# Optimization experiments

Hardware: AMD Instinct MI355X
Metric: run time of the kernel (lower is better)

## Reference

```python
import jax, jax.numpy as jnp
import numpy as np


def patch_merge(x):
    # [B,C,H,W] -> [B,4C,H/2,W/2], channel order [x00, x10, x01, x11]
    x0 = x[:, :, 0::2, 0::2]
    x1 = x[:, :, 1::2, 0::2]
    x2 = x[:, :, 0::2, 1::2]
    x3 = x[:, :, 1::2, 1::2]
    return jnp.concatenate([x0, x1, x2, x3], axis=1)


def patch2image(x):
    # inverse of patch_merge: [B,4C,H,W] -> [B,C,2H,2W]
    B, C4, H, W = x.shape
    C = C4 // 4
    a, b, c, d = x[:, :C], x[:, C:2 * C], x[:, 2 * C:3 * C], x[:, 3 * C:]
    even = jnp.stack([a, c], axis=-1).reshape(B, C, H, 2 * W)  # rows 0::2
    odd = jnp.stack([b, d], axis=-1).reshape(B, C, H, 2 * W)   # rows 1::2
    return jnp.stack([even, odd], axis=-2).reshape(B, C, 2 * H, 2 * W)


def dwconv3x3(x, w, b):
    # depthwise 3x3 conv, SAME padding; w: [C,1,3,3], b: [C]
    C = x.shape[1]
    y = jax.lax.conv_general_dilated(
        x, w, window_strides=(1, 1), padding='SAME',
        dimension_numbers=('NCHW', 'OIHW', 'NCHW'), feature_group_count=C)
    return y + b[None, :, None, None]


def setup_inputs() -> dict:
    key = jax.random.key(0)
    ks = jax.random.split(key, 6)
    B, C, H, W = 8, 32, 256, 256
    x = jax.random.normal(ks[0], (B, C, H, W), dtype=jnp.float32)
    wq = jax.random.normal(ks[1], (C, 1, 3, 3), dtype=jnp.float32) * 0.1
    bq = jax.random.normal(ks[2], (C,), dtype=jnp.float32) * 0.1
    wk = jax.random.normal(ks[3], (C, 1, 3, 3), dtype=jnp.float32) * 0.1
    bk = jax.random.normal(ks[4], (C,), dtype=jnp.float32) * 0.1
    w1 = jax.random.normal(ks[5], (C, C), dtype=jnp.float32) * 0.1  # 1x1 conv, no bias
    return {'x': x, 'wq': wq, 'bq': bq, 'wk': wk, 'bk': bk, 'w1': w1}


def reference(x, wq, bq, wk, bk, w1):
    Q = dwconv3x3(x, wq, bq)
    K = dwconv3x3(x, wk, bk)
    V = x
    for _ in range(4):
        Q = patch_merge(Q)
        K = patch_merge(K)
        V = patch_merge(V)
    b, c, h, w = V.shape
    Qf = Q.reshape(b, c, h * w)
    Kf = K.reshape(b, c, h * w)
    Vf = V.reshape(b, c, h * w)
    # S[b,i,j] = sum_c Q[b,c,i] K[b,c,j]; softmax over j (dim=2)
    S = jax.nn.softmax(jnp.einsum('bci,bcj->bij', Qf, Kf), axis=2)
    # E = V @ S^T
    E = jnp.einsum('bcj,bij->bci', Vf, S).reshape(b, c, h, w)
    for _ in range(4):
        E = patch2image(E)
    E = E + x
    return jnp.einsum('oi,bihw->bohw', w1, E)
```

## Files before the change

### kernel.cpp

```cpp
#include <hip/hip_runtime.h>

#define B_ 8
#define C_ 32
#define NI 256
#define C4 8192

typedef _Float16 f16;
typedef __attribute__((ext_vector_type(8))) _Float16 f16x8;
typedef __attribute__((ext_vector_type(4))) _Float16 f16x4;
typedef __attribute__((ext_vector_type(2))) _Float16 f16x2;
typedef __attribute__((ext_vector_type(4))) float f32x4;

__device__ __forceinline__ int dh_of(int t) { return (t & 1) | ((t >> 1) & 2) | ((t >> 2) & 4) | ((t >> 3) & 8); }
__device__ __forceinline__ int dw_of(int t) { return ((t >> 1) & 1) | ((t >> 2) & 2) | ((t >> 3) & 4) | ((t >> 4) & 8); }
__device__ __forceinline__ int swzu(int u) { return u ^ ((u >> 3) & 7); }

__device__ __forceinline__ void gld16(const void* g, void* lds) {
  __builtin_amdgcn_global_load_lds(
      (const __attribute__((address_space(1))) unsigned int*)g,
      (__attribute__((address_space(3))) unsigned int*)lds, 16, 0, 0);
}

__global__ __launch_bounds__(256) void k1a_conv(
    const float* __restrict__ x, const float* __restrict__ wq, const float* __restrict__ bq,
    const float* __restrict__ wk, const float* __restrict__ bk,
    f16* __restrict__ Qn, f16* __restrict__ Kn, f16* __restrict__ Vtt)
{
  __shared__ __align__(16) float xs[19 * 260];
  const int bid = blockIdx.x;
  const int hi = bid & 15, c = (bid >> 4) & 31, b = bid >> 9;
  const int tid = threadIdx.x;
  const size_t cimg = ((size_t)(b * 32 + c)) << 16;

  if (tid < 19) {
    f32x4 z = {};
    *(f32x4*)&xs[tid * 260 + 256] = z;
  }
#pragma unroll
  for (int s = 0; s < 5; ++s) {
    const int idx = tid + 256 * s;
    if (idx < 1152) {
      const int rr = idx >> 6;
      const int col4 = idx & 63;
      const int gh = hi * 16 - 1 + rr;
      f32x4 v = {};
      if ((unsigned)gh < 256u)
        v = *(const f32x4*)(x + cimg + (size_t)gh * 256 + col4 * 4);
      *(f32x4*)&xs[(rr + 1) * 260 + (swzu(col4) << 2)] = v;
    }
  }
  __syncthreads();

  {
    const int hl = tid >> 4, wseg = tid & 15;
    const int w0 = wseg * 16;
    const int ubase = 4 * wseg - 1;
    float q[16], k[16];
    const float bqv = bq[c], bkv = bk[c];
#pragma unroll
    for (int w = 0; w < 16; ++w) { q[w] = bqv; k[w] = bkv; }
#pragma unroll
    for (int dy = 0; dy < 3; ++dy) {
      const float* row = &xs[(hl + 1 + dy) * 260];
      float rbuf[24];
#pragma unroll
      for (int v6 = 0; v6 < 6; ++v6) {
        const int u = ubase + v6;
        const int off = (u < 0) ? -4 : (u >= 64 ? 256 : (swzu(u) << 2));
        const f32x4 a = *(const f32x4*)(row + off);
#pragma unroll
        for (int e = 0; e < 4; ++e) rbuf[v6 * 4 + e] = a[e];
      }
      const float q0 = wq[c * 9 + dy * 3], q1 = wq[c * 9 + dy * 3 + 1], q2 = wq[c * 9 + dy * 3 + 2];
      const float k0 = wk[c * 9 + dy * 3], k1 = wk[c * 9 + dy * 3 + 1], k2 = wk[c * 9 + dy * 3 + 2];
#pragma unroll
      for (int w = 0; w < 16; ++w) {
        q[w] += rbuf[3 + w] * q0 + rbuf[4 + w] * q1 + rbuf[5 + w] * q2;
        k[w] += rbuf[3 + w] * k0 + rbuf[4 + w] * k1 + rbuf[5 + w] * k2;
      }
    }
    f16x8 qo[2], ko[2];
#pragma unroll
    for (int w = 0; w < 16; ++w) { qo[w >> 3][w & 7] = (f16)q[w]; ko[w >> 3][w & 7] = (f16)k[w]; }
    f16* qp = Qn + cimg + (size_t)(hi * 16 + hl) * 256 + w0;
    f16* kp = Kn + cimg + (size_t)(hi * 16 + hl) * 256 + w0;
    *(f16x8*)qp = qo[0]; *(f16x8*)(qp + 8) = qo[1];
    *(f16x8*)kp = ko[0]; *(f16x8*)(kp + 8) = ko[1];
  }

  {
    const int t = tid;
    const int dh = dh_of(t), dw = dw_of(t);
    const float* rowp = &xs[(dh + 2) * 260];
    f16x8 o0, o1;
#pragma unroll
    for (int wi = 0; wi < 16; ++wi) {
      const int wcol = wi * 16 + dw;
      const f16 v = (f16)rowp[(swzu(wcol >> 2) << 2) | (wcol & 3)];
      if (wi < 8) o0[wi] = v; else o1[wi - 8] = v;
    }
    f16* vdst = Vtt + ((size_t)b * C4 + (size_t)t * 32 + c) * 256 + hi * 16;
    *(f16x8*)vdst = o0;
    *(f16x8*)(vdst + 8) = o1;
  }
}

__global__ __launch_bounds__(256) void k2_logits(
    const f16* __restrict__ Qn, const f16* __restrict__ Kn, float* __restrict__ Spart)
{
  const int b = blockIdx.z;
  const int kt = blockIdx.y;
  const int it = blockIdx.x >> 2, jt = blockIdx.x & 3;
  const int tid = threadIdx.x, wave = tid >> 6, lane = tid & 63;
  const int li = lane & 15, lk = lane >> 4;
  const int i0 = it * 64 + wave * 16;
  const int j0 = jt * 64;
  const f16* Qb = Qn + ((size_t)b << 21);
  const f16* Kb = Kn + ((size_t)b << 21);
  const int dhl = lk >> 1, dwl = (lk & 1) * 8;

  f32x4 acc[4] = {};
  const int kbeg = kt * 2048, kend = kbeg + 2048;
  for (int kk = kbeg; kk < kend; kk += 32) {
    const int c = kk >> 8, dhb = (kk >> 4) & 15;
    const size_t cbase = ((size_t)c << 16) + (size_t)(dhb + dhl) * 256 + li * 16 + dwl;
    const f16x8 a = *(const f16x8*)(Qb + cbase + (size_t)i0 * 256);
#pragma unroll
    for (int jj = 0; jj < 4; ++jj) {
      const f16x8 bb = *(const f16x8*)(Kb + cbase + (size_t)(j0 + jj * 16) * 256);
      acc[jj] = __builtin_amdgcn_mfma_f32_16x16x32_f16(a, bb, acc[jj], 0, 0, 0);
    }
  }
  float* Sp = Spart + ((size_t)kt * B_ + b) * NI * NI;
#pragma unroll
  for (int jj = 0; jj < 4; ++jj)
#pragma unroll
    for (int r = 0; r < 4; ++r) {
      const int ii = i0 + lk * 4 + r;
      const int jc = j0 + jj * 16 + li;
      Sp[(size_t)ii * NI + jc] = acc[jj][r];
    }
}

__global__ __launch_bounds__(256) void k3_softmax(
    const float* __restrict__ Spart, f16* __restrict__ Sh)
{
  const int row = blockIdx.x * 4 + (threadIdx.x >> 6);
  const int lane = threadIdx.x & 63;
  const size_t base = (size_t)row * NI + lane * 4;
  f32x4 v = {0.f, 0.f, 0.f, 0.f};
#pragma unroll
  for (int kt = 0; kt < 4; ++kt) {
    const f32x4 p = *(const f32x4*)(Spart + (size_t)kt * B_ * NI * NI + base);
    v[0] += p[0]; v[1] += p[1]; v[2] += p[2]; v[3] += p[3];
  }
  float m = fmaxf(fmaxf(v[0], v[1]), fmaxf(v[2], v[3]));
#pragma unroll
  for (int d = 1; d < 64; d <<= 1) m = fmaxf(m, __shfl_xor(m, d, 64));
  const float e0 = expf(v[0] - m), e1 = expf(v[1] - m), e2 = expf(v[2] - m), e3 = expf(v[3] - m);
  float s = e0 + e1 + e2 + e3;
#pragma unroll
  for (int d = 1; d < 64; d <<= 1) s += __shfl_xor(s, d, 64);
  const float inv = 1.f / s;
  f16x4 o;
  o[0] = (f16)(e0 * inv); o[1] = (f16)(e1 * inv); o[2] = (f16)(e2 * inv); o[3] = (f16)(e3 * inv);
  *(f16x4*)(Sh + (size_t)row * NI + lane * 4) = o;
}

__global__ __launch_bounds__(256) void k4_ev(
    const f16* __restrict__ Vtt, const f16* __restrict__ Sh, f16* __restrict__ Y)
{
  __shared__ __align__(16) f16 As[128 * 64];
  __shared__ __align__(16) f16 Bs[128 * 64];
  const int mt = blockIdx.x, nt = blockIdx.y, b = blockIdx.z;
  const int m0 = mt * 128, n0 = nt * 128;
  const int tid = threadIdx.x, wave = tid >> 6, lane = tid & 63;
  const int li = lane & 15, lk = lane >> 4;
  const int wm = wave >> 1, wn = wave & 1;
  const f16* Va  = Vtt + (size_t)b * C4 * NI;
  const f16* Shb = Sh + (size_t)b * NI * NI;

  const int srow = tid >> 3, scol = (tid & 7) * 8;

  f32x4 acc[4][4] = {};

#define K4_STAGE(k0)                                                          \
  {                                                                           \
    _Pragma("unroll")                                                         \
    for (int j = 0; j < 4; ++j) {                                             \
      const int rg = j * 32 + srow;                                           \
      gld16(Va + (size_t)(m0 + rg) * NI + (k0) + scol,                        \
            (char*)As + j * 4096 + wave * 1024);                              \
      gld16(Shb + (size_t)(n0 + rg) * NI + (k0) + scol,                       \
            (char*)Bs + j * 4096 + wave * 1024);                              \
    }                                                                         \
  }

  K4_STAGE(0);
#pragma unroll
  for (int kt = 0; kt < 4; ++kt) {
    __syncthreads();
#pragma unroll
    for (int kh = 0; kh < 2; ++kh) {
      f16x8 af[4], bf[4];
#pragma unroll
      for (int mi = 0; mi < 4; ++mi)
        af[mi] = *(const f16x8*)&As[(wm * 64 + mi * 16 + li) * 64 + kh * 32 + lk * 8];
#pragma unroll
      for (int ni = 0; ni < 4; ++ni)
        bf[ni] = *(const f16x8*)&Bs[(wn * 64 + ni * 16 + li) * 64 + kh * 32 + lk * 8];
#pragma unroll
      for (int mi = 0; mi < 4; ++mi)
#pragma unroll
        for (int ni = 0; ni < 4; ++ni)
          acc[mi][ni] = __builtin_amdgcn_mfma_f32_16x16x32_f16(af[mi], bf[ni], acc[mi][ni], 0, 0, 0);
    }
    __syncthreads();
    if (kt < 3) K4_STAGE((kt + 1) * 64);
  }
#undef K4_STAGE

#pragma unroll
  for (int mi = 0; mi < 4; ++mi)
#pragma unroll
    for (int ni = 0; ni < 4; ++ni) {
      const int i = n0 + wn * 64 + ni * 16 + li;
      const int m = m0 + wm * 64 + mi * 16 + lk * 4;
      const f16* vres = Va + (size_t)m * NI + i;
      f16x4 p;
#pragma unroll
      for (int r = 0; r < 4; ++r)
        p[r] = (f16)(acc[mi][ni][r] + (float)vres[(size_t)r * NI]);
      *(f16x4*)(Y + ((size_t)(b * NI + i)) * C4 + m) = p;
    }
}

__global__ __launch_bounds__(256) void k5_w1_unpermute(
    const f16* __restrict__ Y, const float* __restrict__ w1, float* __restrict__ out)
{
  __shared__ f16 w1s[32 * 32];
  const int bid = blockIdx.x;
  const int b = bid >> 8, i = bid & 255;
  const int hi = i >> 4, wi = i & 15;
  const int tid = threadIdx.x;
#pragma unroll
  for (int e = 0; e < 4; ++e) w1s[tid + 256 * e] = (f16)w1[tid + 256 * e];
  __syncthreads();

  const int wave = tid >> 6, lane = tid & 63, li = lane & 15, lk = lane >> 4;
  const f16* Yrow = Y + ((size_t)(b * NI + i)) * C4;
  const f16x8 b0 = *(const f16x8*)(&w1s[li * 32 + lk * 8]);
  const f16x8 b1 = *(const f16x8*)(&w1s[(16 + li) * 32 + lk * 8]);

#pragma unroll
  for (int q = 0; q < 4; ++q) {
    const int tt = wave * 4 + q;
    const f16x8 a = *(const f16x8*)(Yrow + (size_t)(tt * 16 + li) * 32 + lk * 8);
    f32x4 d0 = {}, d1 = {};
    d0 = __builtin_amdgcn_mfma_f32_16x16x32_f16(a, b0, d0, 0, 0, 0);
    d1 = __builtin_amdgcn_mfma_f32_16x16x32_f16(a, b1, d1, 0, 0, 0);
#pragma unroll
    for (int r = 0; r < 4; ++r) {
      const int t = tt * 16 + lk * 4 + r;
      const int dh = dh_of(t), dw = dw_of(t);
      const int h = hi * 16 + dh, w = wi * 16 + dw;
      out[(((size_t)(b * 32 + li)) * 256 + h) * 256 + w] = d0[r];
      out[(((size_t)(b * 32 + 16 + li)) * 256 + h) * 256 + w] = d1[r];
    }
  }
}

extern "C" void kernel_launch(void* const* d_in, const int* in_sizes, int n_in,
                              void* d_out, int out_size, void* d_ws, size_t ws_size,
                              hipStream_t stream)
{
  const float* x  = (const float*)d_in[0];
  const float* wq = (const float*)d_in[1];
  const float* bq = (const float*)d_in[2];
  const float* wk = (const float*)d_in[3];
  const float* bk = (const float*)d_in[4];
  const float* w1 = (const float*)d_in[5];
  float* out = (float*)d_out;
  char* ws = (char*)d_ws;

  f16*   Qn    = (f16*)(ws);
  f16*   Kn    = (f16*)(ws + 33554432);
  f16*   Vtt   = (f16*)(ws + 67108864);
  float* Spart = (float*)(ws + 100663296);
  f16*   Sh    = (f16*)(ws + 109051904);
  f16*   Y     = Qn;

  k1a_conv<<<4096, 256, 0, stream>>>(x, wq, bq, wk, bk, Qn, Kn, Vtt);
  k2_logits<<<dim3(16, 4, 8), 256, 0, stream>>>(Qn, Kn, Spart);
  k3_softmax<<<512, 256, 0, stream>>>(Spart, Sh);
  k4_ev<<<dim3(64, 2, 8), 256, 0, stream>>>(Vtt, Sh, Y);
  k5_w1_unpermute<<<2048, 256, 0, stream>>>(Y, w1, out);
}
```

Before: 136.4 us.

## Stage logits GEMM tiles in LDS via direct global-to-LDS loads

Rewrites the QK^T logits kernel so each block loads 64x64 Q and 128x64 K tiles into shared memory with global_load_lds. Each wave then computes a 32x64 sub-tile from LDS instead of reading K fragments straight from global memory. The split-K factor goes from 4 to 8, so the softmax kernel now sums eight partial slices and the Sh buffer moves to a later offset. The aim is more operand reuse and less redundant global traffic, at the cost of extra partial-sum writes and reads and two barriers per k-step with no double buffering.

```diff
diff --git a/kernel.cpp b/kernel.cpp
--- a/kernel.cpp
+++ b/kernel.cpp
@@ -108,38 +108,78 @@
 __global__ __launch_bounds__(256) void k2_logits(
     const f16* __restrict__ Qn, const f16* __restrict__ Kn, float* __restrict__ Spart)
 {
-  const int b = blockIdx.z;
-  const int kt = blockIdx.y;
-  const int it = blockIdx.x >> 2, jt = blockIdx.x & 3;
+  __shared__ __align__(16) f16 As[64 * 64];
+  __shared__ __align__(16) f16 Bs[128 * 64];
+  const int tile = blockIdx.x;
+  const int mt = tile >> 1, nt = tile & 1;
+  const int kz = blockIdx.y, b = blockIdx.z;
+  const int i0 = mt * 64, j0 = nt * 128;
   const int tid = threadIdx.x, wave = tid >> 6, lane = tid & 63;
   const int li = lane & 15, lk = lane >> 4;
-  const int i0 = it * 64 + wave * 16;
-  const int j0 = jt * 64;
+  const int wm = wave >> 1, wn = wave & 1;
   const f16* Qb = Qn + ((size_t)b << 21);
   const f16* Kb = Kn + ((size_t)b << 21);
-  const int dhl = lk >> 1, dwl = (lk & 1) * 8;
-
-  f32x4 acc[4] = {};
-  const int kbeg = kt * 2048, kend = kbeg + 2048;
-  for (int kk = kbeg; kk < kend; kk += 32) {
-    const int c = kk >> 8, dhb = (kk >> 4) & 15;
-    const size_t cbase = ((size_t)c << 16) + (size_t)(dhb + dhl) * 256 + li * 16 + dwl;
-    const f16x8 a = *(const f16x8*)(Qb + cbase + (size_t)i0 * 256);
-#pragma unroll
-    for (int jj = 0; jj < 4; ++jj) {
-      const f16x8 bb = *(const f16x8*)(Kb + cbase + (size_t)(j0 + jj * 16) * 256);
-      acc[jj] = __builtin_amdgcn_mfma_f32_16x16x32_f16(a, bb, acc[jj], 0, 0, 0);
-    }
-  }
-  float* Sp = Spart + ((size_t)kt * B_ + b) * NI * NI;
-#pragma unroll
-  for (int jj = 0; jj < 4; ++jj)
-#pragma unroll
-    for (int r = 0; r < 4; ++r) {
-      const int ii = i0 + lk * 4 + r;
-      const int jc = j0 + jj * 16 + li;
-      Sp[(size_t)ii * NI + jc] = acc[jj][r];
-    }
+  const int srow = tid >> 3, scol8 = (tid & 7) * 8;
+
+  f32x4 acc[2][4] = {};
+
+#define K2_RADDR(r) ((((size_t)((r) >> 4)) << 12) + (size_t)((r) & 15) * 16)
+#define K2_STAGE(kk)                                                          \
+  {                                                                           \
+    const int c_ = (kk) >> 8, dhb_ = ((kk) >> 4) & 15;                        \
+    const size_t kpart = ((size_t)c_ << 16) +                                 \
+        (size_t)(dhb_ + (scol8 >> 4)) * 256 + (scol8 & 8);                    \
+    _Pragma("unroll")                                                         \
+    for (int j = 0; j < 2; ++j) {                                             \
+      const int rg = j * 32 + srow;                                           \
+      gld16(Qb + kpart + K2_RADDR(i0 + rg),                                   \
+            (char*)As + j * 4096 + wave * 1024);                              \
+    }                                                                         \
+    _Pragma("unroll")                                                         \
+    for (int j = 0; j < 4; ++j) {                                             \
+      const int rg = j * 32 + srow;                                           \
+      gld16(Kb + kpart + K2_RADDR(j0 + rg),                                   \
+            (char*)Bs + j * 4096 + wave * 1024);                              \
+    }                                                                         \
+  }
+
+  const int kbase = kz * 1024;
+  K2_STAGE(kbase);
+#pragma unroll
+  for (int kt = 0; kt < 16; ++kt) {
+    __syncthreads();
+#pragma unroll
+    for (int kh = 0; kh < 2; ++kh) {
+      f16x8 af[2], bf[4];
+#pragma unroll
+      for (int mi = 0; mi < 2; ++mi)
+        af[mi] = *(const f16x8*)&As[(wm * 32 + mi * 16 + li) * 64 + kh * 32 + lk * 8];
+#pragma unroll
+      for (int ni = 0; ni < 4; ++ni)
+        bf[ni] = *(const f16x8*)&Bs[(wn * 64 + ni * 16 + li) * 64 + kh * 32 + lk * 8];
+#pragma unroll
+      for (int mi = 0; mi < 2; ++mi)
+#pragma unroll
+        for (int ni = 0; ni < 4; ++ni)
+          acc[mi][ni] = __builtin_amdgcn_mfma_f32_16x16x32_f16(af[mi], bf[ni], acc[mi][ni], 0, 0, 0);
+    }
+    __syncthreads();
+    if (kt < 15) K2_STAGE(kbase + (kt + 1) * 64);
+  }
+#undef K2_STAGE
+#undef K2_RADDR
+
+  float* Sp = Spart + ((size_t)kz * B_ + b) * NI * NI;
+#pragma unroll
+  for (int mi = 0; mi < 2; ++mi)
+#pragma unroll
+    for (int ni = 0; ni < 4; ++ni)
+#pragma unroll
+      for (int r = 0; r < 4; ++r) {
+        const int ii = i0 + wm * 32 + mi * 16 + lk * 4 + r;
+        const int jc = j0 + wn * 64 + ni * 16 + li;
+        Sp[(size_t)ii * NI + jc] = acc[mi][ni][r];
+      }
 }
 
 __global__ __launch_bounds__(256) void k3_softmax(
@@ -150,7 +190,7 @@
   const size_t base = (size_t)row * NI + lane * 4;
   f32x4 v = {0.f, 0.f, 0.f, 0.f};
 #pragma unroll
-  for (int kt = 0; kt < 4; ++kt) {
+  for (int kt = 0; kt < 8; ++kt) {
     const f32x4 p = *(const f32x4*)(Spart + (size_t)kt * B_ * NI * NI + base);
     v[0] += p[0]; v[1] += p[1]; v[2] += p[2]; v[3] += p[3];
   }
@@ -287,11 +327,11 @@
   f16*   Kn    = (f16*)(ws + 33554432);
   f16*   Vtt   = (f16*)(ws + 67108864);
   float* Spart = (float*)(ws + 100663296);
-  f16*   Sh    = (f16*)(ws + 109051904);
+  f16*   Sh    = (f16*)(ws + 117440512);
   f16*   Y     = Qn;
 
   k1a_conv<<<4096, 256, 0, stream>>>(x, wq, bq, wk, bk, Qn, Kn, Vtt);
-  k2_logits<<<dim3(16, 4, 8), 256, 0, stream>>>(Qn, Kn, Spart);
+  k2_logits<<<dim3(8, 8, 8), 256, 0, stream>>>(Qn, Kn, Spart);
   k3_softmax<<<512, 256, 0, stream>>>(Spart, Sh);
   k4_ev<<<dim3(64, 2, 8), 256, 0, stream>>>(Vtt, Sh, Y);
   k5_w1_unpermute<<<2048, 256, 0, stream>>>(Y, w1, out);
```

Result: no change. 136.7 us (+0.2%).
